# Optimization experiments

Measured on AMD Instinct MI355X. Metric: run time of the kernel, lower is better.

Reference implementation:

```python
import jax, jax.numpy as jnp
import numpy as np

MAX_ITERS = 4096  # safety cap; original loops until convergence (expected ~235 iters here)
COS_EPS = 1e-8    # torch F.cosine_similarity denominator clamp


def fire_neurons(x, b, q, e):
    """Vectorized GLS chaotic firing. x:(B,N); b,q,e:(N,). Returns k:(B,N).

    Faithful to the torch loop: m starts at q, each iteration applies the skew-tent
    map to ALL elements; an element stays 'active' while it has been outside
    [x-e, x+e] in every iteration so far (intersection chain), and k counts
    1 + number of iterations it stayed active. Elements with q==0 never fire.
    """
    m0 = jnp.broadcast_to(q, x.shape).astype(x.dtype)
    k0 = jnp.ones_like(x)
    act0 = m0 != 0  # torch.nonzero(m[idx]) seeds the active set
    lo = x - e
    hi = x + e

    def cond(state):
        i, m, k, act = state
        return jnp.logical_and(act.any(), i < MAX_ITERS)

    def body(state):
        i, m, k, act = state
        m = jnp.where(m < b, m / b, (1.0 - m) / (1.0 - b))  # skew-tent GLS map
        invalid = (m < lo) | (m > hi)
        act = act & invalid                                  # np.intersect1d(invalid, last)
        k = k + act.astype(k.dtype)
        return (i + 1, m, k, act)

    _, _, k, _ = jax.lax.while_loop(cond, body, (jnp.int32(0), m0, k0, act0))
    return k


def cosine_logits(k, M):
    """Row-wise cosine similarity of each firing pattern k[i]:(N,) vs each class row M[c]:(N,)."""
    kn = jnp.maximum(jnp.linalg.norm(k, axis=1), COS_EPS)  # (B,)
    Mn = jnp.maximum(jnp.linalg.norm(M, axis=1), COS_EPS)  # (C,)
    return (k @ M.T) / (kn[:, None] * Mn[None, :])          # (B,C)


def setup_inputs() -> dict:
    key = jax.random.key(0)
    kx, kb, kq, ke, kM = jax.random.split(key, 5)
    B, N, C = 256, 8192, 100
    x = jax.random.uniform(kx, (B, N), dtype=jnp.float32)              # inputs in (0,1)
    b = 0.25 + 0.5 * jax.random.uniform(kb, (N,), dtype=jnp.float32)   # map break in (0.25,0.75)
    q = 0.02 + 0.96 * jax.random.uniform(kq, (N,), dtype=jnp.float32)  # nonzero init potential
    e = 0.03 + 0.03 * jax.random.uniform(ke, (N,), dtype=jnp.float32)  # epsilon in (0.03,0.06)
    M = jax.random.uniform(kM, (C, N), dtype=jnp.float32)              # class prototypes (post-train)
    return {"x": x, "b": b, "q": q, "e": e, "M": M}


def reference(x, b, q, e, M):
    # forward(x, return_logits=True): fire neurons, then per-sample cosine similarity vs M
    k = fire_neurons(x, b, q, e)
    return cosine_logits(k, M)
```

## Files before the change

kernel.cpp:

```cpp
#include <hip/hip_runtime.h>
#include <math.h>

#define NN 8192
#define BB 256
#define CC 100
#define MAX_ITERS 4096
#define CHUNK 10

__global__ __launch_bounds__(256) void fire_kernel(
    const float* __restrict__ x, const float* __restrict__ bmap,
    const float* __restrict__ qini, const float* __restrict__ eps,
    float* __restrict__ kout)
{
    const int j    = blockIdx.x;
    const int lane = threadIdx.x & 63;
    const int row  = (threadIdx.x & ~63) + lane;

    const float bv  = bmap[j];
    const float qv  = qini[j];
    const float ev  = eps[j];
    const float obv = 1.0f - bv;
    const float rb  = 1.0f / bv;
    const float rob = 1.0f / obv;

    const float xv  = x[(size_t)row * NN + j];
    const float lov = xv - ev;
    const float hiv = xv + ev;

    float m = qv, anchor = qv;
    int   window = 1, steps = 0;
    int   kk = 1;
    bool  a  = (qv != 0.0f);
    bool  cycseen = false;

    int it = 0;
    while (it < MAX_ITERS) {
        #pragma unroll
        for (int u = 0; u < 4; ++u) {
            const bool  lt = (m < bv);
            const float pa = m * rb;
            const float pb = (1.0f - m) * rob;
            m = lt ? pa : pb;

            cycseen = cycseen || (m == anchor);
            if (++steps == window) { anchor = m; window <<= 1; steps = 0; }

            const bool o = (m < lov) || (m > hiv);
            a = a && o;
            kk += a ? 1 : 0;
        }
        it += 4;
        if (__ballot(a) == 0ull) break;
        if (cycseen) {
            kk += a ? (MAX_ITERS - it) : 0;
            break;
        }
    }

    kout[(size_t)row * NN + j] = (float)kk;
}

__global__ __launch_bounds__(256) void logits_kernel(
    const float* __restrict__ k, const float* __restrict__ M,
    float* __restrict__ out)
{
    __shared__ float  redd[4][4];
    __shared__ double redm[4];
    __shared__ double redk[4][4];
    __shared__ float  knsh[4];

    const int rq  = blockIdx.x / CHUNK;
    const int ch  = blockIdx.x % CHUNK;
    const int i0  = rq * 4;
    const int tid = threadIdx.x;
    const int wid = tid >> 6, lane = tid & 63;

    float4 kr[4][8];
    #pragma unroll
    for (int r = 0; r < 4; ++r)
        #pragma unroll
        for (int s = 0; s < 8; ++s)
            kr[r][s] = *(const float4*)(k + (size_t)(i0 + r) * NN + s * 1024 + tid * 4);

    {
        double ks[4] = {0.0, 0.0, 0.0, 0.0};
        #pragma unroll
        for (int s = 0; s < 8; ++s)
            #pragma unroll
            for (int r = 0; r < 4; ++r) {
                const float4 v = kr[r][s];
                ks[r] += (double)v.x * v.x + (double)v.y * v.y
                       + (double)v.z * v.z + (double)v.w * v.w;
            }
        #pragma unroll
        for (int off = 32; off; off >>= 1)
            #pragma unroll
            for (int r = 0; r < 4; ++r) ks[r] += __shfl_down(ks[r], off, 64);
        if (lane == 0)
            #pragma unroll
            for (int r = 0; r < 4; ++r) redk[wid][r] = ks[r];
        __syncthreads();
        if (tid < 4) {
            const double t = redk[0][tid] + redk[1][tid] + redk[2][tid] + redk[3][tid];
            knsh[tid] = fmaxf((float)sqrt(t), 1e-8f);
        }
        __syncthreads();
    }

    for (int c = ch * CHUNK; c < ch * CHUNK + CHUNK; ++c) {
        const float4* Mp = (const float4*)(M + (size_t)c * NN);
        float  acc[4] = {0.0f, 0.0f, 0.0f, 0.0f};
        double msq = 0.0;
        #pragma unroll
        for (int s = 0; s < 8; ++s) {
            const float4 mv = Mp[s * 256 + tid];
            msq += (double)mv.x * mv.x + (double)mv.y * mv.y
                 + (double)mv.z * mv.z + (double)mv.w * mv.w;
            #pragma unroll
            for (int r = 0; r < 4; ++r)
                acc[r] += kr[r][s].x * mv.x + kr[r][s].y * mv.y
                        + kr[r][s].z * mv.z + kr[r][s].w * mv.w;
        }
        #pragma unroll
        for (int off = 32; off; off >>= 1) {
            #pragma unroll
            for (int r = 0; r < 4; ++r) acc[r] += __shfl_down(acc[r], off, 64);
            msq += __shfl_down(msq, off, 64);
        }
        if (lane == 0) {
            #pragma unroll
            for (int r = 0; r < 4; ++r) redd[wid][r] = acc[r];
            redm[wid] = msq;
        }
        __syncthreads();
        if (tid < 4) {
            const double mt = redm[0] + redm[1] + redm[2] + redm[3];
            const float  mn = fmaxf((float)sqrt(mt), 1e-8f);
            const float  d  = redd[0][tid] + redd[1][tid] + redd[2][tid] + redd[3][tid];
            out[(size_t)(i0 + tid) * CC + c] = d / (knsh[tid] * mn);
        }
        __syncthreads();
    }
}

__global__ __launch_bounds__(256) void gls_fused_kernel(
    const float* __restrict__ x, const float* __restrict__ bmap,
    const float* __restrict__ qini, const float* __restrict__ eps,
    const float* __restrict__ M, float* __restrict__ out)
{
    __shared__ float k_lds[NN];
    __shared__ double redsh[4];

    const int i   = blockIdx.x;
    const int tid = threadIdx.x;
    const int wid = tid >> 6, lane = tid & 63;

    double sumsq = 0.0;
    for (int s = 0; s < 32; ++s) {
        const int j = tid + 256 * s;
        const float bv = bmap[j];
        const float qv = qini[j];
        const float ev = eps[j];
        const float xv = x[(size_t)i * NN + j];
        const float lov = xv - ev;
        const float hiv = xv + ev;
        const float obv = 1.0f - bv;
        const float rb  = 1.0f / bv;
        const float rob = 1.0f / obv;

        float m  = qv;
        float kk = 1.0f;
        bool  a  = (qv != 0.0f);
        for (int it = 0; a && it < MAX_ITERS; ++it) {
            const bool  lt  = (m < bv);
            const float num = lt ? m  : (1.0f - m);
            const float r   = lt ? rb : rob;
            m = num * r;
            a = (m < lov) || (m > hiv);
            kk += a ? 1.0f : 0.0f;
        }
        k_lds[j] = kk;
        sumsq += (double)kk * (double)kk;
    }

    #pragma unroll
    for (int off = 32; off; off >>= 1) sumsq += __shfl_down(sumsq, off, 64);
    if (lane == 0) redsh[wid] = sumsq;
    __syncthreads();
    const double rn = fmax(sqrt(redsh[0] + redsh[1] + redsh[2] + redsh[3]), 1e-8);

    for (int cc2 = 0; cc2 < 25; ++cc2) {
        const int c = wid * 25 + cc2;
        const float4* Mp = (const float4*)(M + (size_t)c * NN);
        double dot = 0.0, msq = 0.0;
        #pragma unroll 4
        for (int s = 0; s < 32; ++s) {
            const float4 mv = Mp[lane + 64 * s];
            const float4 kv = *(const float4*)(&k_lds[4 * (lane + 64 * s)]);
            dot += (double)kv.x * (double)mv.x + (double)kv.y * (double)mv.y
                 + (double)kv.z * (double)mv.z + (double)kv.w * (double)mv.w;
            msq += (double)mv.x * (double)mv.x + (double)mv.y * (double)mv.y
                 + (double)mv.z * (double)mv.z + (double)mv.w * (double)mv.w;
        }
        #pragma unroll
        for (int off = 32; off; off >>= 1) {
            dot += __shfl_down(dot, off, 64);
            msq += __shfl_down(msq, off, 64);
        }
        if (lane == 0) {
            const double mn = fmax(sqrt(msq), 1e-8);
            out[(size_t)i * CC + c] = (float)(dot / (rn * mn));
        }
    }
}

extern "C" void kernel_launch(void* const* d_in, const int* in_sizes, int n_in,
                              void* d_out, int out_size, void* d_ws, size_t ws_size,
                              hipStream_t stream) {
    const float* x = (const float*)d_in[0];
    const float* b = (const float*)d_in[1];
    const float* q = (const float*)d_in[2];
    const float* e = (const float*)d_in[3];
    const float* M = (const float*)d_in[4];
    float* out = (float*)d_out;

    const size_t need = (size_t)BB * NN * sizeof(float);
    if (ws_size >= need) {
        float* kbuf = (float*)d_ws;
        fire_kernel<<<dim3(NN), dim3(256), 0, stream>>>(x, b, q, e, kbuf);
        logits_kernel<<<dim3((BB / 4) * CHUNK), dim3(256), 0, stream>>>(kbuf, M, out);
    } else {
        gls_fused_kernel<<<dim3(BB), dim3(256), 0, stream>>>(x, b, q, e, M, out);
    }
}
```

Before: 117.4 us.

## Split firing into capped first pass plus work-list pass for long-running wavefronts

The firing kernel now stops each wavefront after a capped number of iterations. Wavefronts that are still active are pushed onto a global work list through an atomic counter, and a second kernel with many small blocks finishes them. This targets load imbalance, where a few slow wavefronts hold 256-thread blocks resident until they finish. A separate kernel also precomputes the M row norms once, instead of recomputing them in every logits block. The cost is extra kernel launches, atomics, and a list that caps at a fixed size before falling back to inline iteration.

```diff
diff --git a/kernel.cpp b/kernel.cpp
--- a/kernel.cpp
+++ b/kernel.cpp
@@ -5,16 +5,22 @@
 #define BB 256
 #define CC 100
 #define MAX_ITERS 4096
+#define T0CAP 384
+#define LISTMAX 4096
 #define CHUNK 10
 
-__global__ __launch_bounds__(256) void fire_kernel(
+__global__ void zero_kernel(unsigned* __restrict__ cnt) { *cnt = 0u; }
+
+__global__ __launch_bounds__(256) void fireA_kernel(
     const float* __restrict__ x, const float* __restrict__ bmap,
     const float* __restrict__ qini, const float* __restrict__ eps,
-    float* __restrict__ kout)
+    float* __restrict__ kout, unsigned* __restrict__ cnt,
+    unsigned* __restrict__ list)
 {
     const int j    = blockIdx.x;
     const int lane = threadIdx.x & 63;
-    const int row  = (threadIdx.x & ~63) + lane;
+    const int wg   = threadIdx.x >> 6;
+    const int row  = wg * 64 + lane;
 
     const float bv  = bmap[j];
     const float qv  = qini[j];
@@ -32,40 +38,136 @@
     int   kk = 1;
     bool  a  = (qv != 0.0f);
     bool  cycseen = false;
+    bool  finished = false;
 
     int it = 0;
-    while (it < MAX_ITERS) {
+    while (it < T0CAP) {
         #pragma unroll
         for (int u = 0; u < 4; ++u) {
             const bool  lt = (m < bv);
             const float pa = m * rb;
             const float pb = (1.0f - m) * rob;
             m = lt ? pa : pb;
-
             cycseen = cycseen || (m == anchor);
             if (++steps == window) { anchor = m; window <<= 1; steps = 0; }
-
             const bool o = (m < lov) || (m > hiv);
             a = a && o;
             kk += a ? 1 : 0;
         }
         it += 4;
-        if (__ballot(a) == 0ull) break;
-        if (cycseen) {
-            kk += a ? (MAX_ITERS - it) : 0;
-            break;
+        if (__ballot(a) == 0ull) { finished = true; break; }
+        if (cycseen) { kk += a ? (MAX_ITERS - it) : 0; finished = true; break; }
+    }
+
+    if (!finished) {
+        unsigned idx = 0;
+        if (lane == 0) idx = atomicAdd(cnt, 1u);
+        idx = (unsigned)__shfl((int)idx, 0, 64);
+        if (idx < LISTMAX) {
+            if (lane == 0) list[idx] = ((unsigned)j << 2) | (unsigned)wg;
+            return;
+        }
+        while (it < MAX_ITERS) {
+            #pragma unroll
+            for (int u = 0; u < 4; ++u) {
+                const bool  lt = (m < bv);
+                const float pa = m * rb;
+                const float pb = (1.0f - m) * rob;
+                m = lt ? pa : pb;
+                cycseen = cycseen || (m == anchor);
+                if (++steps == window) { anchor = m; window <<= 1; steps = 0; }
+                const bool o = (m < lov) || (m > hiv);
+                a = a && o;
+                kk += a ? 1 : 0;
+            }
+            it += 4;
+            if (__ballot(a) == 0ull) break;
+            if (cycseen) { kk += a ? (MAX_ITERS - it) : 0; break; }
         }
     }
 
     kout[(size_t)row * NN + j] = (float)kk;
+}
+
+__global__ __launch_bounds__(64) void fireB_kernel(
+    const float* __restrict__ x, const float* __restrict__ bmap,
+    const float* __restrict__ qini, const float* __restrict__ eps,
+    float* __restrict__ kout, const unsigned* __restrict__ cnt,
+    const unsigned* __restrict__ list)
+{
+    const unsigned n = min(*cnt, (unsigned)LISTMAX);
+    const int lane = threadIdx.x;
+
+    for (unsigned idx = blockIdx.x; idx < n; idx += gridDim.x) {
+        const unsigned ent = list[idx];
+        const int j   = (int)(ent >> 2);
+        const int row = (int)(ent & 3u) * 64 + lane;
+
+        const float bv  = bmap[j];
+        const float qv  = qini[j];
+        const float ev  = eps[j];
+        const float obv = 1.0f - bv;
+        const float rb  = 1.0f / bv;
+        const float rob = 1.0f / obv;
+
+        const float xv  = x[(size_t)row * NN + j];
+        const float lov = xv - ev;
+        const float hiv = xv + ev;
+
+        float m = qv, anchor = qv;
+        int   window = 1, steps = 0;
+        int   kk = 1;
+        bool  a  = (qv != 0.0f);
+        bool  cycseen = false;
+
+        int it = 0;
+        while (it < MAX_ITERS) {
+            #pragma unroll
+            for (int u = 0; u < 4; ++u) {
+                const bool  lt = (m < bv);
+                const float pa = m * rb;
+                const float pb = (1.0f - m) * rob;
+                m = lt ? pa : pb;
+                cycseen = cycseen || (m == anchor);
+                if (++steps == window) { anchor = m; window <<= 1; steps = 0; }
+                const bool o = (m < lov) || (m > hiv);
+                a = a && o;
+                kk += a ? 1 : 0;
+            }
+            it += 4;
+            if (__ballot(a) == 0ull) break;
+            if (cycseen) { kk += a ? (MAX_ITERS - it) : 0; break; }
+        }
+
+        kout[(size_t)row * NN + j] = (float)kk;
+    }
+}
+
+__global__ __launch_bounds__(256) void normM_kernel(
+    const float* __restrict__ M, float* __restrict__ Mn)
+{
+    __shared__ double red[4];
+    const float* src = M + (size_t)blockIdx.x * NN;
+    double s = 0.0;
+    for (int j = threadIdx.x * 4; j < NN; j += 1024) {
+        const float4 v = *(const float4*)(src + j);
+        s += (double)v.x * v.x + (double)v.y * v.y
+           + (double)v.z * v.z + (double)v.w * v.w;
+    }
+    #pragma unroll
+    for (int off = 32; off; off >>= 1) s += __shfl_down(s, off, 64);
+    const int wid = threadIdx.x >> 6, lane = threadIdx.x & 63;
+    if (lane == 0) red[wid] = s;
+    __syncthreads();
+    if (threadIdx.x == 0)
+        Mn[blockIdx.x] = fmaxf((float)sqrt(red[0] + red[1] + red[2] + red[3]), 1e-8f);
 }
 
 __global__ __launch_bounds__(256) void logits_kernel(
     const float* __restrict__ k, const float* __restrict__ M,
-    float* __restrict__ out)
+    const float* __restrict__ Mn, float* __restrict__ out)
 {
     __shared__ float  redd[4][4];
-    __shared__ double redm[4];
     __shared__ double redk[4][4];
     __shared__ float  knsh[4];
 
@@ -109,35 +211,26 @@
 
     for (int c = ch * CHUNK; c < ch * CHUNK + CHUNK; ++c) {
         const float4* Mp = (const float4*)(M + (size_t)c * NN);
-        float  acc[4] = {0.0f, 0.0f, 0.0f, 0.0f};
-        double msq = 0.0;
+        float acc[4] = {0.0f, 0.0f, 0.0f, 0.0f};
         #pragma unroll
         for (int s = 0; s < 8; ++s) {
             const float4 mv = Mp[s * 256 + tid];
-            msq += (double)mv.x * mv.x + (double)mv.y * mv.y
-                 + (double)mv.z * mv.z + (double)mv.w * mv.w;
             #pragma unroll
             for (int r = 0; r < 4; ++r)
                 acc[r] += kr[r][s].x * mv.x + kr[r][s].y * mv.y
                         + kr[r][s].z * mv.z + kr[r][s].w * mv.w;
         }
         #pragma unroll
-        for (int off = 32; off; off >>= 1) {
+        for (int off = 32; off; off >>= 1)
             #pragma unroll
             for (int r = 0; r < 4; ++r) acc[r] += __shfl_down(acc[r], off, 64);
-            msq += __shfl_down(msq, off, 64);
-        }
-        if (lane == 0) {
+        if (lane == 0)
             #pragma unroll
             for (int r = 0; r < 4; ++r) redd[wid][r] = acc[r];
-            redm[wid] = msq;
-        }
         __syncthreads();
         if (tid < 4) {
-            const double mt = redm[0] + redm[1] + redm[2] + redm[3];
-            const float  mn = fmaxf((float)sqrt(mt), 1e-8f);
-            const float  d  = redd[0][tid] + redd[1][tid] + redd[2][tid] + redd[3][tid];
-            out[(size_t)(i0 + tid) * CC + c] = d / (knsh[tid] * mn);
+            const float d = redd[0][tid] + redd[1][tid] + redd[2][tid] + redd[3][tid];
+            out[(size_t)(i0 + tid) * CC + c] = d / (knsh[tid] * Mn[c]);
         }
         __syncthreads();
     }
@@ -224,11 +317,21 @@
     const float* M = (const float*)d_in[4];
     float* out = (float*)d_out;
 
-    const size_t need = (size_t)BB * NN * sizeof(float);
-    if (ws_size >= need) {
-        float* kbuf = (float*)d_ws;
-        fire_kernel<<<dim3(NN), dim3(256), 0, stream>>>(x, b, q, e, kbuf);
-        logits_kernel<<<dim3((BB / 4) * CHUNK), dim3(256), 0, stream>>>(kbuf, M, out);
+    const size_t kbytes    = (size_t)BB * NN * sizeof(float);
+    const size_t need_full = kbytes + CC * sizeof(float) + 64
+                           + sizeof(unsigned) * (LISTMAX + 1);
+
+    if (ws_size >= need_full) {
+        float*    kbuf = (float*)d_ws;
+        float*    Mn   = kbuf + (size_t)BB * NN;
+        unsigned* cnt  = (unsigned*)((char*)d_ws + kbytes + CC * sizeof(float));
+        unsigned* list = cnt + 1;
+
+        zero_kernel<<<dim3(1), dim3(1), 0, stream>>>(cnt);
+        fireA_kernel<<<dim3(NN), dim3(256), 0, stream>>>(x, b, q, e, kbuf, cnt, list);
+        fireB_kernel<<<dim3(512), dim3(64), 0, stream>>>(x, b, q, e, kbuf, cnt, list);
+        normM_kernel<<<dim3(CC), dim3(256), 0, stream>>>(M, Mn);
+        logits_kernel<<<dim3((BB / 4) * CHUNK), dim3(256), 0, stream>>>(kbuf, M, Mn, out);
     } else {
         gls_fused_kernel<<<dim3(BB), dim3(256), 0, stream>>>(x, b, q, e, M, out);
     }
```

Result: slower. 158.5 us (+35.0%).
